# Optimization experiments

Measured on AMD Instinct MI355X. Metric: run time of the kernel, lower is better.

## Reference

```python
import jax, jax.numpy as jnp
import numpy as np

N = 100000
E = 1600000
IN_DIM, HID_DIM, OUT_DIM = 128, 64, 32


def setup_inputs() -> dict:
    key = jax.random.key(0)
    k1, k2, k3, k4, k5, k6 = jax.random.split(key, 6)
    x = jax.random.normal(k1, (N, IN_DIM), dtype=jnp.float32)
    edge_index = jax.random.randint(k2, (2, E), 0, N, dtype=jnp.int64)
    # Glorot-ish init for GCN weights
    W1 = jax.random.normal(k3, (IN_DIM, HID_DIM), dtype=jnp.float32) / np.sqrt(IN_DIM)
    b1 = jnp.zeros((HID_DIM,), dtype=jnp.float32)
    W2 = jax.random.normal(k4, (HID_DIM, OUT_DIM), dtype=jnp.float32) / np.sqrt(HID_DIM)
    b2 = jnp.zeros((OUT_DIM,), dtype=jnp.float32)
    return {"x": x, "edge_index": edge_index, "W1": W1, "b1": b1, "W2": W2, "b2": b2}


def _gcn_norm(edge_index, num_nodes):
    # add self loops, compute symmetric normalization coefficients
    loop = jnp.arange(num_nodes, dtype=edge_index.dtype)
    row = jnp.concatenate([edge_index[0], loop])  # source
    col = jnp.concatenate([edge_index[1], loop])  # target
    deg = jax.ops.segment_sum(jnp.ones_like(col, dtype=jnp.float32), col,
                              num_segments=num_nodes)
    dinv = jax.lax.rsqrt(deg)  # deg >= 1 due to self loops
    norm = dinv[row] * dinv[col]  # [E+N]
    return row, col, norm


def _gcn_conv(x, W, b, row, col, norm, num_nodes):
    h = x @ W                       # [N, out]
    msg = h[row] * norm[:, None]    # gather + scale  [E+N, out]
    out = jax.ops.segment_sum(msg, col, num_segments=num_nodes)  # scatter-add
    return out + b


def reference(x, edge_index, W1, b1, W2, b2):
    num_nodes = x.shape[0]
    row, col, norm = _gcn_norm(edge_index, num_nodes)
    h = _gcn_conv(x, W1, b1, row, col, norm, num_nodes)
    h = jax.nn.relu(h)
    # dropout(p=0.6) is identity in eval mode
    out = _gcn_conv(h, W2, b2, row, col, norm, num_nodes)
    return out
```

## Files before the change

### kernel.cpp

```cpp
#include <hip/hip_runtime.h>


#define NNODES 100000
#define NEDGES 1600000
#define IN_DIM 128
#define HID 64
#define OUTD 32

#define BKT_NODES 128
#define NBUK 782
#define BKT_CAP 3584
#define P1_BLOCKS 256
#define P1_CHUNK (NEDGES / P1_BLOCKS)


__global__ __launch_bounds__(256) void k_pass1(const int* __restrict__ row,
                                               const int* __restrict__ col,
                                               int* __restrict__ gcur,
                                               int2* __restrict__ pairbuf) {
    __shared__ int lcnt[NBUK];
    __shared__ int lbase[NBUK];
    int t = threadIdx.x;
    int e0 = blockIdx.x * P1_CHUNK;
    int e1 = e0 + P1_CHUNK;
    for (int j = t; j < NBUK; j += 256) lcnt[j] = 0;
    __syncthreads();
    for (int e = e0 + t; e < e1; e += 256)
        atomicAdd(&lcnt[col[e] >> 7], 1);
    __syncthreads();
    for (int j = t; j < NBUK; j += 256) {
        int n = lcnt[j];
        lbase[j] = (n > 0) ? atomicAdd(&gcur[j], n) : 0;
    }
    __syncthreads();
    for (int j = t; j < NBUK; j += 256) lcnt[j] = 0;
    __syncthreads();
    for (int e = e0 + t; e < e1; e += 256) {
        int c = col[e];
        int r = row[e];
        int b = c >> 7;
        int pos = lbase[b] + atomicAdd(&lcnt[b], 1);
        if (pos < BKT_CAP) pairbuf[(size_t)b * BKT_CAP + pos] = make_int2(c, r);
    }
}

__global__ __launch_bounds__(1024) void k_bktscan(const int* __restrict__ gcur,
                                                  int* __restrict__ bktbase,
                                                  int* __restrict__ ptr) {
    __shared__ int s[1024];
    int t = threadIdx.x;
    int v = (t < NBUK) ? gcur[t] : 0;
    s[t] = v;
    __syncthreads();
    for (int off = 1; off < 1024; off <<= 1) {
        int u = (t >= off) ? s[t - off] : 0;
        __syncthreads();
        s[t] += u;
        __syncthreads();
    }
    if (t < NBUK) bktbase[t] = s[t] - v;
    if (t == 0) { bktbase[NBUK] = NEDGES; ptr[NNODES] = NEDGES; }
}

__global__ __launch_bounds__(256) void k_pass2(const int2* __restrict__ pairbuf,
                                               const int* __restrict__ gcur,
                                               const int* __restrict__ bktbase,
                                               int* __restrict__ ptr,
                                               float* __restrict__ dinv,
                                               int* __restrict__ adj) {
    __shared__ int ncnt[BKT_NODES];
    __shared__ int nsc[BKT_NODES];
    __shared__ int ncur[BKT_NODES];
    __shared__ int seg[BKT_CAP];
    int b = blockIdx.x;
    int t = threadIdx.x;
    int c0 = b * BKT_NODES;
    int nb = NNODES - c0; if (nb > BKT_NODES) nb = BKT_NODES;
    int size = gcur[b]; if (size > BKT_CAP) size = BKT_CAP;
    int base = bktbase[b];
    const int2* pp = pairbuf + (size_t)b * BKT_CAP;

    if (t < BKT_NODES) ncnt[t] = 0;
    __syncthreads();
    for (int k = t; k < size; k += 256)
        atomicAdd(&ncnt[pp[k].x - c0], 1);
    __syncthreads();
    int myv = (t < BKT_NODES) ? ncnt[t] : 0;
    if (t < BKT_NODES) nsc[t] = myv;
    __syncthreads();
    for (int off = 1; off < BKT_NODES; off <<= 1) {
        int u = 0;
        if (t < BKT_NODES && t >= off) u = nsc[t - off];
        __syncthreads();
        if (t < BKT_NODES) nsc[t] += u;
        __syncthreads();
    }
    if (t < BKT_NODES) {
        int excl = nsc[t] - myv;
        ncur[t] = excl;
        if (t < nb) {
            ptr[c0 + t] = base + excl;
            dinv[c0 + t] = rsqrtf((float)myv + 1.0f);
        }
    }
    __syncthreads();
    for (int k = t; k < size; k += 256) {
        int2 pr = pp[k];
        int pos = atomicAdd(&ncur[pr.x - c0], 1);
        seg[pos] = pr.y;
    }
    __syncthreads();
    for (int k = t; k < size; k += 256) adj[base + k] = seg[k];
}


#define TILE 64
#define NT 16
__global__ __launch_bounds__(256) void k_gemm1(const float* __restrict__ x,
                                               const float* __restrict__ W1,
                                               const float* __restrict__ dinv,
                                               float* __restrict__ g1) {
    __shared__ float shx[TILE][IN_DIM];
    int t = threadIdx.x;
    int nbase = blockIdx.x * TILE;

    const float4* xg = reinterpret_cast<const float4*>(x + (size_t)nbase * IN_DIM);
    float4* shx4 = reinterpret_cast<float4*>(&shx[0][0]);
    int lim = (NNODES - nbase) * (IN_DIM / 4);
    if (lim > TILE * (IN_DIM / 4)) lim = TILE * (IN_DIM / 4);
#pragma unroll
    for (int it = 0; it < 8; ++it) {
        int idx = t + it * 256;
        if (idx < lim) shx4[idx] = xg[idx];
    }
    __syncthreads();

    int w = t >> 6;
    int lane = t & 63;
    int n0 = w * NT;

    float acc[NT];
#pragma unroll
    for (int n = 0; n < NT; ++n) acc[n] = 0.0f;

    for (int kc = 0; kc < IN_DIM / 4; ++kc) {
        float w0 = W1[(kc * 4 + 0) * HID + lane];
        float w1 = W1[(kc * 4 + 1) * HID + lane];
        float w2 = W1[(kc * 4 + 2) * HID + lane];
        float w3 = W1[(kc * 4 + 3) * HID + lane];
#pragma unroll
        for (int n = 0; n < NT; ++n) {
            float4 xv = *reinterpret_cast<const float4*>(&shx[n0 + n][kc * 4]);
            acc[n] = fmaf(xv.x, w0, acc[n]);
            acc[n] = fmaf(xv.y, w1, acc[n]);
            acc[n] = fmaf(xv.z, w2, acc[n]);
            acc[n] = fmaf(xv.w, w3, acc[n]);
        }
    }
#pragma unroll
    for (int n = 0; n < NT; ++n) {
        int node = nbase + n0 + n;
        if (node < NNODES)
            g1[(size_t)node * HID + lane] = dinv[node] * acc[n];
    }
}

__global__ __launch_bounds__(256) void k_agg1g2(const float* __restrict__ g1,
                                                const int* __restrict__ ptr,
                                                const int* __restrict__ adj,
                                                const float* __restrict__ dinv,
                                                const float* __restrict__ b1,
                                                const float* __restrict__ W2,
                                                float* __restrict__ g2) {
    __shared__ float sh[4][HID];
    int t = blockIdx.x * blockDim.x + threadIdx.x;
    int i = t >> 6;
    if (i >= NNODES) return;
    int lane = threadIdx.x & 63;
    int w = threadIdx.x >> 6;

    float s = g1[(size_t)i * HID + lane];
    int p0 = ptr[i], p1 = ptr[i + 1];
    int p = p0;
    for (; p + 8 <= p1; p += 8) {
        int n0 = adj[p],     n1 = adj[p + 1], n2 = adj[p + 2], n3 = adj[p + 3];
        int n4 = adj[p + 4], n5 = adj[p + 5], n6 = adj[p + 6], n7 = adj[p + 7];
        float v0 = g1[(size_t)n0 * HID + lane];
        float v1 = g1[(size_t)n1 * HID + lane];
        float v2 = g1[(size_t)n2 * HID + lane];
        float v3 = g1[(size_t)n3 * HID + lane];
        float v4 = g1[(size_t)n4 * HID + lane];
        float v5 = g1[(size_t)n5 * HID + lane];
        float v6 = g1[(size_t)n6 * HID + lane];
        float v7 = g1[(size_t)n7 * HID + lane];
        s += ((v0 + v1) + (v2 + v3)) + ((v4 + v5) + (v6 + v7));
    }
    for (; p < p1; ++p) s += g1[(size_t)adj[p] * HID + lane];

    float di = dinv[i];
    float h = fmaxf(fmaf(di, s, b1[lane]), 0.0f);
    sh[w][lane] = h;

    int j2 = lane & 31;
    int half = lane >> 5;
    float acc = 0.0f;
#pragma unroll
    for (int j = 0; j < 32; ++j) {
        int jj = half * 32 + j;
        acc = fmaf(sh[w][jj], W2[jj * OUTD + j2], acc);
    }
    acc += __shfl_xor(acc, 32);
    if (half == 0) g2[(size_t)i * OUTD + j2] = di * acc;
}

__global__ void k_agg2(const float* __restrict__ g2, const int* __restrict__ ptr,
                       const int* __restrict__ adj, const float* __restrict__ dinv,
                       const float* __restrict__ b2, float* __restrict__ out) {
    int t = blockIdx.x * blockDim.x + threadIdx.x;
    int i = t >> 5;
    int j = t & 31;
    if (i >= NNODES) return;
    float s = g2[(size_t)i * OUTD + j];
    int p0 = ptr[i], p1 = ptr[i + 1];
    int p = p0;
    for (; p + 8 <= p1; p += 8) {
        int n0 = adj[p],     n1 = adj[p + 1], n2 = adj[p + 2], n3 = adj[p + 3];
        int n4 = adj[p + 4], n5 = adj[p + 5], n6 = adj[p + 6], n7 = adj[p + 7];
        float v0 = g2[(size_t)n0 * OUTD + j];
        float v1 = g2[(size_t)n1 * OUTD + j];
        float v2 = g2[(size_t)n2 * OUTD + j];
        float v3 = g2[(size_t)n3 * OUTD + j];
        float v4 = g2[(size_t)n4 * OUTD + j];
        float v5 = g2[(size_t)n5 * OUTD + j];
        float v6 = g2[(size_t)n6 * OUTD + j];
        float v7 = g2[(size_t)n7 * OUTD + j];
        s += ((v0 + v1) + (v2 + v3)) + ((v4 + v5) + (v6 + v7));
    }
    for (; p < p1; ++p) s += g2[(size_t)adj[p] * OUTD + j];
    out[(size_t)i * OUTD + j] = fmaf(dinv[i], s, b2[j]);
}

extern "C" void kernel_launch(void* const* d_in, const int* in_sizes, int n_in,
                              void* d_out, int out_size, void* d_ws, size_t ws_size,
                              hipStream_t stream) {
    const float* x  = (const float*)d_in[0];
    const int*   ei = (const int*)d_in[1];
    const float* W1 = (const float*)d_in[2];
    const float* b1 = (const float*)d_in[3];
    const float* W2 = (const float*)d_in[4];
    const float* b2 = (const float*)d_in[5];
    float* out = (float*)d_out;

    const int* row = ei;
    const int* col = ei + NEDGES;

    char* ws = (char*)d_ws;
    size_t off = 0;
    auto alloc = [&](size_t bytes) {
        void* p = ws + off;
        off = (off + bytes + 511) & ~(size_t)511;
        return p;
    };
    int*   gcur    = (int*)  alloc((size_t)NBUK * 4);
    int*   bktbase = (int*)  alloc((size_t)(NBUK + 1) * 4);
    int*   ptr     = (int*)  alloc((size_t)(NNODES + 1) * 4);
    float* dinv    = (float*)alloc((size_t)NNODES * 4);
    int*   adj     = (int*)  alloc((size_t)NEDGES * 4);
    float* g2      = (float*)alloc((size_t)NNODES * OUTD * 4);
    size_t big = (size_t)NBUK * BKT_CAP * 8;
    size_t g1b = (size_t)NNODES * HID * 4;
    int2*  pairbuf = (int2*) alloc(big > g1b ? big : g1b);
    float* g1      = (float*)pairbuf;

    const int B = 256;
    hipMemsetAsync(gcur, 0, (size_t)NBUK * 4, stream);
    k_pass1<<<P1_BLOCKS, 256, 0, stream>>>(row, col, gcur, pairbuf);
    k_bktscan<<<1, 1024, 0, stream>>>(gcur, bktbase, ptr);
    k_pass2<<<NBUK, 256, 0, stream>>>(pairbuf, gcur, bktbase, ptr, dinv, adj);

    {
        int nblk = (NNODES + TILE - 1) / TILE;
        k_gemm1<<<nblk, 256, 0, stream>>>(x, W1, dinv, g1);
    }
    {
        long long tot = (long long)NNODES * HID;
        k_agg1g2<<<(int)((tot + B - 1) / B), B, 0, stream>>>(g1, ptr, adj, dinv, b1, W2, g2);
    }
    {
        long long tot = (long long)NNODES * OUTD;
        k_agg2<<<(int)((tot + B - 1) / B), B, 0, stream>>>(g2, ptr, adj, dinv, b2, out);
    }
}
```

Measured before the change: 301.2 us.

## Store intermediate features in fp16 and pack edge pairs into one word

The intermediate node features g1 and g2 are now stored as fp16 instead of fp32, which halves the bytes moved by the random neighbour gathers in both aggregation kernels. The bucket sort's pair buffer now holds one packed 32-bit word per edge (source id shifted left by 7, OR'd with the low 7 bits of the target) instead of an int2, halving that traffic as well. Accumulation is still done in fp32, but the stored features lose precision, which may affect accuracy tolerance.

```diff
diff --git a/kernel.cpp b/kernel.cpp
--- a/kernel.cpp
+++ b/kernel.cpp
@@ -1,4 +1,5 @@
 #include <hip/hip_runtime.h>
+#include <hip/hip_fp16.h>
 
 
 #define NNODES 100000
@@ -17,7 +18,7 @@
 __global__ __launch_bounds__(256) void k_pass1(const int* __restrict__ row,
                                                const int* __restrict__ col,
                                                int* __restrict__ gcur,
-                                               int2* __restrict__ pairbuf) {
+                                               unsigned int* __restrict__ pairbuf) {
     __shared__ int lcnt[NBUK];
     __shared__ int lbase[NBUK];
     int t = threadIdx.x;
@@ -37,10 +38,10 @@
     __syncthreads();
     for (int e = e0 + t; e < e1; e += 256) {
         int c = col[e];
-        int r = row[e];
+        unsigned int pk = ((unsigned int)row[e] << 7) | (unsigned int)(c & 127);
         int b = c >> 7;
         int pos = lbase[b] + atomicAdd(&lcnt[b], 1);
-        if (pos < BKT_CAP) pairbuf[(size_t)b * BKT_CAP + pos] = make_int2(c, r);
+        if (pos < BKT_CAP) pairbuf[(size_t)b * BKT_CAP + pos] = pk;
     }
 }
 
@@ -62,7 +63,7 @@
     if (t == 0) { bktbase[NBUK] = NEDGES; ptr[NNODES] = NEDGES; }
 }
 
-__global__ __launch_bounds__(256) void k_pass2(const int2* __restrict__ pairbuf,
+__global__ __launch_bounds__(256) void k_pass2(const unsigned int* __restrict__ pairbuf,
                                                const int* __restrict__ gcur,
                                                const int* __restrict__ bktbase,
                                                int* __restrict__ ptr,
@@ -78,12 +79,12 @@
     int nb = NNODES - c0; if (nb > BKT_NODES) nb = BKT_NODES;
     int size = gcur[b]; if (size > BKT_CAP) size = BKT_CAP;
     int base = bktbase[b];
-    const int2* pp = pairbuf + (size_t)b * BKT_CAP;
+    const unsigned int* pp = pairbuf + (size_t)b * BKT_CAP;
 
     if (t < BKT_NODES) ncnt[t] = 0;
     __syncthreads();
     for (int k = t; k < size; k += 256)
-        atomicAdd(&ncnt[pp[k].x - c0], 1);
+        atomicAdd(&ncnt[pp[k] & 127u], 1);
     __syncthreads();
     int myv = (t < BKT_NODES) ? ncnt[t] : 0;
     if (t < BKT_NODES) nsc[t] = myv;
@@ -105,9 +106,9 @@
     }
     __syncthreads();
     for (int k = t; k < size; k += 256) {
-        int2 pr = pp[k];
-        int pos = atomicAdd(&ncur[pr.x - c0], 1);
-        seg[pos] = pr.y;
+        unsigned int pk = pp[k];
+        int pos = atomicAdd(&ncur[pk & 127u], 1);
+        seg[pos] = (int)(pk >> 7);
     }
     __syncthreads();
     for (int k = t; k < size; k += 256) adj[base + k] = seg[k];
@@ -119,7 +120,7 @@
 __global__ __launch_bounds__(256) void k_gemm1(const float* __restrict__ x,
                                                const float* __restrict__ W1,
                                                const float* __restrict__ dinv,
-                                               float* __restrict__ g1) {
+                                               __half* __restrict__ g1) {
     __shared__ float shx[TILE][IN_DIM];
     int t = threadIdx.x;
     int nbase = blockIdx.x * TILE;
@@ -161,17 +162,17 @@
     for (int n = 0; n < NT; ++n) {
         int node = nbase + n0 + n;
         if (node < NNODES)
-            g1[(size_t)node * HID + lane] = dinv[node] * acc[n];
-    }
-}
-
-__global__ __launch_bounds__(256) void k_agg1g2(const float* __restrict__ g1,
+            g1[(size_t)node * HID + lane] = __float2half(dinv[node] * acc[n]);
+    }
+}
+
+__global__ __launch_bounds__(256) void k_agg1g2(const __half* __restrict__ g1,
                                                 const int* __restrict__ ptr,
                                                 const int* __restrict__ adj,
                                                 const float* __restrict__ dinv,
                                                 const float* __restrict__ b1,
                                                 const float* __restrict__ W2,
-                                                float* __restrict__ g2) {
+                                                __half* __restrict__ g2) {
     __shared__ float sh[4][HID];
     int t = blockIdx.x * blockDim.x + threadIdx.x;
     int i = t >> 6;
@@ -179,23 +180,23 @@
     int lane = threadIdx.x & 63;
     int w = threadIdx.x >> 6;
 
-    float s = g1[(size_t)i * HID + lane];
+    float s = __half2float(g1[(size_t)i * HID + lane]);
     int p0 = ptr[i], p1 = ptr[i + 1];
     int p = p0;
     for (; p + 8 <= p1; p += 8) {
         int n0 = adj[p],     n1 = adj[p + 1], n2 = adj[p + 2], n3 = adj[p + 3];
         int n4 = adj[p + 4], n5 = adj[p + 5], n6 = adj[p + 6], n7 = adj[p + 7];
-        float v0 = g1[(size_t)n0 * HID + lane];
-        float v1 = g1[(size_t)n1 * HID + lane];
-        float v2 = g1[(size_t)n2 * HID + lane];
-        float v3 = g1[(size_t)n3 * HID + lane];
-        float v4 = g1[(size_t)n4 * HID + lane];
-        float v5 = g1[(size_t)n5 * HID + lane];
-        float v6 = g1[(size_t)n6 * HID + lane];
-        float v7 = g1[(size_t)n7 * HID + lane];
+        float v0 = __half2float(g1[(size_t)n0 * HID + lane]);
+        float v1 = __half2float(g1[(size_t)n1 * HID + lane]);
+        float v2 = __half2float(g1[(size_t)n2 * HID + lane]);
+        float v3 = __half2float(g1[(size_t)n3 * HID + lane]);
+        float v4 = __half2float(g1[(size_t)n4 * HID + lane]);
+        float v5 = __half2float(g1[(size_t)n5 * HID + lane]);
+        float v6 = __half2float(g1[(size_t)n6 * HID + lane]);
+        float v7 = __half2float(g1[(size_t)n7 * HID + lane]);
         s += ((v0 + v1) + (v2 + v3)) + ((v4 + v5) + (v6 + v7));
     }
-    for (; p < p1; ++p) s += g1[(size_t)adj[p] * HID + lane];
+    for (; p < p1; ++p) s += __half2float(g1[(size_t)adj[p] * HID + lane]);
 
     float di = dinv[i];
     float h = fmaxf(fmaf(di, s, b1[lane]), 0.0f);
@@ -210,33 +211,33 @@
         acc = fmaf(sh[w][jj], W2[jj * OUTD + j2], acc);
     }
     acc += __shfl_xor(acc, 32);
-    if (half == 0) g2[(size_t)i * OUTD + j2] = di * acc;
-}
-
-__global__ void k_agg2(const float* __restrict__ g2, const int* __restrict__ ptr,
+    if (half == 0) g2[(size_t)i * OUTD + j2] = __float2half(di * acc);
+}
+
+__global__ void k_agg2(const __half* __restrict__ g2, const int* __restrict__ ptr,
                        const int* __restrict__ adj, const float* __restrict__ dinv,
                        const float* __restrict__ b2, float* __restrict__ out) {
     int t = blockIdx.x * blockDim.x + threadIdx.x;
     int i = t >> 5;
     int j = t & 31;
     if (i >= NNODES) return;
-    float s = g2[(size_t)i * OUTD + j];
+    float s = __half2float(g2[(size_t)i * OUTD + j]);
     int p0 = ptr[i], p1 = ptr[i + 1];
     int p = p0;
     for (; p + 8 <= p1; p += 8) {
         int n0 = adj[p],     n1 = adj[p + 1], n2 = adj[p + 2], n3 = adj[p + 3];
         int n4 = adj[p + 4], n5 = adj[p + 5], n6 = adj[p + 6], n7 = adj[p + 7];
-        float v0 = g2[(size_t)n0 * OUTD + j];
-        float v1 = g2[(size_t)n1 * OUTD + j];
-        float v2 = g2[(size_t)n2 * OUTD + j];
-        float v3 = g2[(size_t)n3 * OUTD + j];
-        float v4 = g2[(size_t)n4 * OUTD + j];
-        float v5 = g2[(size_t)n5 * OUTD + j];
-        float v6 = g2[(size_t)n6 * OUTD + j];
-        float v7 = g2[(size_t)n7 * OUTD + j];
+        float v0 = __half2float(g2[(size_t)n0 * OUTD + j]);
+        float v1 = __half2float(g2[(size_t)n1 * OUTD + j]);
+        float v2 = __half2float(g2[(size_t)n2 * OUTD + j]);
+        float v3 = __half2float(g2[(size_t)n3 * OUTD + j]);
+        float v4 = __half2float(g2[(size_t)n4 * OUTD + j]);
+        float v5 = __half2float(g2[(size_t)n5 * OUTD + j]);
+        float v6 = __half2float(g2[(size_t)n6 * OUTD + j]);
+        float v7 = __half2float(g2[(size_t)n7 * OUTD + j]);
         s += ((v0 + v1) + (v2 + v3)) + ((v4 + v5) + (v6 + v7));
     }
-    for (; p < p1; ++p) s += g2[(size_t)adj[p] * OUTD + j];
+    for (; p < p1; ++p) s += __half2float(g2[(size_t)adj[p] * OUTD + j]);
     out[(size_t)i * OUTD + j] = fmaf(dinv[i], s, b2[j]);
 }
 
@@ -261,16 +262,16 @@
         off = (off + bytes + 511) & ~(size_t)511;
         return p;
     };
-    int*   gcur    = (int*)  alloc((size_t)NBUK * 4);
-    int*   bktbase = (int*)  alloc((size_t)(NBUK + 1) * 4);
-    int*   ptr     = (int*)  alloc((size_t)(NNODES + 1) * 4);
-    float* dinv    = (float*)alloc((size_t)NNODES * 4);
-    int*   adj     = (int*)  alloc((size_t)NEDGES * 4);
-    float* g2      = (float*)alloc((size_t)NNODES * OUTD * 4);
-    size_t big = (size_t)NBUK * BKT_CAP * 8;
-    size_t g1b = (size_t)NNODES * HID * 4;
-    int2*  pairbuf = (int2*) alloc(big > g1b ? big : g1b);
-    float* g1      = (float*)pairbuf;
+    int*    gcur    = (int*)   alloc((size_t)NBUK * 4);
+    int*    bktbase = (int*)   alloc((size_t)(NBUK + 1) * 4);
+    int*    ptr     = (int*)   alloc((size_t)(NNODES + 1) * 4);
+    float*  dinv    = (float*) alloc((size_t)NNODES * 4);
+    int*    adj     = (int*)   alloc((size_t)NEDGES * 4);
+    __half* g2      = (__half*)alloc((size_t)NNODES * OUTD * 2);
+    size_t big = (size_t)NBUK * BKT_CAP * 4;
+    size_t g1b = (size_t)NNODES * HID * 2;
+    unsigned int* pairbuf = (unsigned int*)alloc(big > g1b ? big : g1b);
+    __half* g1 = (__half*)pairbuf;
 
     const int B = 256;
     hipMemsetAsync(gcur, 0, (size_t)NBUK * 4, stream);
```

New measurement: 300.6 us. About the same (-0.2%).
